# Kernel optimization log

Measured on AMD Instinct MI355X. Metric: run time of the kernel, lower is better.

Reference implementation:

```python
import jax, jax.numpy as jnp
import numpy as np

N = 50000      # nodes
E = 800000     # edges (avg degree 16)
D = 64         # num_node_features
H = 64         # hidden_channels
G = 512        # graphs in batch
OUT = 32       # final linear output
NEG_SLOPE = 0.2


def setup_inputs() -> dict:
    key = jax.random.key(0)
    ks = jax.random.split(key, 20)
    s = 0.1  # param init scale
    inp = {
        "x": jax.random.normal(ks[0], (N, D), jnp.float32),
        "edge_index": jax.random.randint(ks[1], (2, E), 0, N, dtype=jnp.int64),
        "batch": jnp.sort(jax.random.randint(ks[2], (N,), 0, G, dtype=jnp.int64)),
        # GATv2 layer 1 (D -> H)
        "Wl1": jax.random.normal(ks[3], (D, H), jnp.float32) * s,
        "bl1": jnp.zeros((H,), jnp.float32),
        "Wr1": jax.random.normal(ks[4], (D, H), jnp.float32) * s,
        "br1": jnp.zeros((H,), jnp.float32),
        "att1": jax.random.normal(ks[5], (H,), jnp.float32) * s,
        "bias1": jnp.zeros((H,), jnp.float32),
        # GATv2 layer 2 (H -> H)
        "Wl2": jax.random.normal(ks[6], (H, H), jnp.float32) * s,
        "bl2": jnp.zeros((H,), jnp.float32),
        "Wr2": jax.random.normal(ks[7], (H, H), jnp.float32) * s,
        "br2": jnp.zeros((H,), jnp.float32),
        "att2": jax.random.normal(ks[8], (H,), jnp.float32) * s,
        "bias2": jnp.zeros((H,), jnp.float32),
        # final classifier
        "lin_w": jax.random.normal(ks[9], (H, OUT), jnp.float32) * s,
        "lin_b": jnp.zeros((OUT,), jnp.float32),
    }
    return inp


def _gatv2(x, src, dst, Wl, bl, Wr, br, att, bias):
    # GATv2Conv, heads=1, PyG semantics: messages flow src -> dst
    xl = x @ Wl + bl                       # [N, H] source transform (also the message)
    xr = x @ Wr + br                       # [N, H] destination transform
    z = xl[src] + xr[dst]                  # [E, H] gather
    e = jax.nn.leaky_relu(z, NEG_SLOPE) @ att  # [E] edge scores
    # segment softmax over edges grouped by destination node
    m = jax.ops.segment_max(e, dst, num_segments=N)   # [N]
    ex = jnp.exp(e - m[dst])                          # [E]
    denom = jax.ops.segment_sum(ex, dst, num_segments=N)  # [N]
    alpha = ex / denom[dst]                            # [E]
    out = jax.ops.segment_sum(alpha[:, None] * xl[src], dst, num_segments=N)  # [N, H]
    return out + bias


def reference(x, edge_index, batch,
              Wl1, bl1, Wr1, br1, att1, bias1,
              Wl2, bl2, Wr2, br2, att2, bias2,
              lin_w, lin_b):
    src, dst = edge_index[0], edge_index[1]
    h = jax.nn.relu(_gatv2(x, src, dst, Wl1, bl1, Wr1, br1, att1, bias1))
    h = jax.nn.relu(_gatv2(h, src, dst, Wl2, bl2, Wr2, br2, att2, bias2))
    # global mean pool over graphs
    sums = jax.ops.segment_sum(h, batch, num_segments=G)          # [G, H]
    cnts = jax.ops.segment_sum(jnp.ones((h.shape[0],), h.dtype), batch, num_segments=G)
    pooled = sums / jnp.maximum(cnts, 1.0)[:, None]
    # dropout(p=0.5) is identity at inference
    return pooled @ lin_w + lin_b                                  # [G, 32]
```

## Files before the change

### kernel.cpp

```cpp
#include <hip/hip_runtime.h>
#include <hip/hip_fp16.h>
#include <math.h>


#define ELLC    48
#define OVF_CAP 65536
#define ECHUNK  2048

typedef int      vint4 __attribute__((ext_vector_type(4)));
typedef _Float16 half4 __attribute__((ext_vector_type(4)));

#define GROWS 32
__device__ __forceinline__ void dual_gemm_slim(
    int bid, int t,
    const float* __restrict__ X,
    const float* __restrict__ Wl, const float* __restrict__ bl,
    const float* __restrict__ Wr, const float* __restrict__ br,
    _Float16* __restrict__ xl, float* __restrict__ xr, int n,
    float* xS) {
    int row0 = bid * GROWS;
    for (int i = t; i < GROWS * 16; i += 256) {
        int r = row0 + (i >> 4);
        float4 v = make_float4(0.f, 0.f, 0.f, 0.f);
        if (r < n) v = ((const float4*)(X + (size_t)r * 64))[i & 15];
        ((float4*)xS)[i] = v;
    }
    __syncthreads();
    int h  = t & 63;
    int rb = t >> 6;
    float accl[8], accr[8];
#pragma unroll
    for (int i = 0; i < 8; ++i) { accl[i] = 0.f; accr[i] = 0.f; }
#pragma unroll 4
    for (int d = 0; d < 64; ++d) {
        float wl = Wl[d * 64 + h];
        float wr = Wr[d * 64 + h];
#pragma unroll
        for (int i = 0; i < 8; ++i) {
            float xv = xS[(rb + 4 * i) * 64 + d];
            accl[i] += xv * wl;
            accr[i] += xv * wr;
        }
    }
    float blv = bl[h], brv = br[h];
#pragma unroll
    for (int i = 0; i < 8; ++i) {
        int r = row0 + rb + 4 * i;
        if (r < n) {
            xl[(size_t)r * 64 + h] = (_Float16)(accl[i] + blv);
            xr[(size_t)r * 64 + h] = accr[i] + brv;
        }
    }
}

__global__ __launch_bounds__(256) void dual_gemm64_kernel(
    const float* __restrict__ X,
    const float* __restrict__ Wl, const float* __restrict__ bl,
    const float* __restrict__ Wr, const float* __restrict__ br,
    _Float16* __restrict__ xl, float* __restrict__ xr, int n) {
    __shared__ float xS[GROWS * 64];
    dual_gemm_slim(blockIdx.x, threadIdx.x, X, Wl, bl, Wr, br, xl, xr, n, xS);
}

__global__ __launch_bounds__(256) void fill_gemm_kernel(
    const int* __restrict__ src, const int* __restrict__ dst,
    int* __restrict__ cnt, unsigned short* __restrict__ ell,
    int* __restrict__ novf, int* __restrict__ ovf_dst, int* __restrict__ ovf_src,
    int E, int N, int psize, int fb,
    const float* __restrict__ X,
    const float* __restrict__ Wl, const float* __restrict__ bl,
    const float* __restrict__ Wr, const float* __restrict__ br,
    _Float16* __restrict__ xl, float* __restrict__ xr) {
    __shared__ float xS[GROWS * 64];
    int b = blockIdx.x;
    if (b >= fb) {
        dual_gemm_slim(b - fb, threadIdx.x, X, Wl, bl, Wr, br, xl, xr, N, xS);
        return;
    }
    int t     = threadIdx.x;
    int chunk = b >> 3;
    int p     = b & 7;
    int d0    = p * psize;
    int d1    = min(N, d0 + psize);
    int e0    = chunk * ECHUNK;
    int e1    = min(E, e0 + ECHUNK);
    int nq    = (e1 - e0) >> 2;
    const vint4* dst4 = (const vint4*)(dst + e0);
    const vint4* src4 = (const vint4*)(src + e0);

    auto scatter4 = [&](vint4 dv, vint4 sv) {
#pragma unroll
        for (int k = 0; k < 4; ++k) {
            int d = dv[k];
            int s = sv[k];
            if (d >= d0 && d < d1) {
                int pos = atomicAdd(&cnt[d], 1);
                if (pos < ELLC) {
                    ell[d * ELLC + pos] = (unsigned short)s;
                } else {
                    int j = atomicAdd(novf, 1);
                    if (j < OVF_CAP) { ovf_dst[j] = d; ovf_src[j] = s; }
                }
            }
        }
    };

    if (nq == (ECHUNK >> 2)) {
        vint4 dvA = __builtin_nontemporal_load(&dst4[t]);
        vint4 svA = __builtin_nontemporal_load(&src4[t]);
        vint4 dvB = __builtin_nontemporal_load(&dst4[t + 256]);
        vint4 svB = __builtin_nontemporal_load(&src4[t + 256]);
        scatter4(dvA, svA);
        scatter4(dvB, svB);
    } else {
        for (int q = t; q < nq; q += 256) {
            vint4 dv = __builtin_nontemporal_load(&dst4[q]);
            vint4 sv = __builtin_nontemporal_load(&src4[q]);
            scatter4(dv, sv);
        }
        for (int e = e0 + (nq << 2) + t; e < e1; e += 256) {
            int d = dst[e];
            if (d >= d0 && d < d1) {
                int pos = atomicAdd(&cnt[d], 1);
                int s   = src[e];
                if (pos < ELLC) {
                    ell[d * ELLC + pos] = (unsigned short)s;
                } else {
                    int j = atomicAdd(novf, 1);
                    if (j < OVF_CAP) { ovf_dst[j] = d; ovf_src[j] = s; }
                }
            }
        }
    }
}

__global__ __launch_bounds__(256) void gat_aggregate_kernel(
    const _Float16* __restrict__ xl, const float* __restrict__ xr,
    const int* __restrict__ cnt, const unsigned short* __restrict__ ell,
    const int* __restrict__ novf, const int* __restrict__ ovf_dst,
    const int* __restrict__ ovf_src,
    const float* __restrict__ att, const float* __restrict__ bias,
    float* __restrict__ out, int n) {
    int wid  = (blockIdx.x * blockDim.x + threadIdx.x) >> 6;
    int lane = threadIdx.x & 63;
    if (wid >= n) return;
    int g = lane >> 4;
    int l = lane & 15;
    int d = wid;

    float4 att4 = ((const float4*)att)[l];
    float4 b4   = ((const float4*)bias)[l];
    int deg_d = cnt[d];
    int nd  = min(deg_d, ELLC);
    int beg = d * ELLC;

    if (deg_d == 0) {
        if (g == 0) {
            float4 v;
            v.x = fmaxf(b4.x, 0.f); v.y = fmaxf(b4.y, 0.f);
            v.z = fmaxf(b4.z, 0.f); v.w = fmaxf(b4.w, 0.f);
            ((float4*)(out + (size_t)d * 64))[l] = v;
        }
        return;
    }

    int myidx = 0;
    if (lane < ELLC) myidx = (int)ell[beg + lane];
    int i_first = __shfl(myidx, 0);

    float4 xr4 = ((const float4*)(xr + (size_t)d * 64))[l];
    float  s   = 0.f;
    float4 acc = make_float4(0.f, 0.f, 0.f, 0.f);

#pragma unroll 6
    for (int k = 0; k * 8 < nd; ++k) {
        int  sa = k * 8 + g, sb = sa + 4;
        bool aa = sa < nd,   ab = sb < nd;
        int  i0 = __shfl(myidx, sa); if (!aa) i0 = i_first;
        int  i1 = __shfl(myidx, sb); if (!ab) i1 = i_first;
        half4 h0 = ((const half4*)(xl + (size_t)i0 * 64))[l];
        half4 h1 = ((const half4*)(xl + (size_t)i1 * 64))[l];
        float4 x0 = make_float4((float)h0[0], (float)h0[1], (float)h0[2], (float)h0[3]);
        float4 x1 = make_float4((float)h1[0], (float)h1[1], (float)h1[2], (float)h1[3]);
        float z, c0 = 0.f, c1 = 0.f;
        z = x0.x + xr4.x; c0 += ((z > 0.f) ? z : 0.2f * z) * att4.x;
        z = x0.y + xr4.y; c0 += ((z > 0.f) ? z : 0.2f * z) * att4.y;
        z = x0.z + xr4.z; c0 += ((z > 0.f) ? z : 0.2f * z) * att4.z;
        z = x0.w + xr4.w; c0 += ((z > 0.f) ? z : 0.2f * z) * att4.w;
        z = x1.x + xr4.x; c1 += ((z > 0.f) ? z : 0.2f * z) * att4.x;
        z = x1.y + xr4.y; c1 += ((z > 0.f) ? z : 0.2f * z) * att4.y;
        z = x1.z + xr4.z; c1 += ((z > 0.f) ? z : 0.2f * z) * att4.z;
        z = x1.w + xr4.w; c1 += ((z > 0.f) ? z : 0.2f * z) * att4.w;
#pragma unroll
        for (int sh = 8; sh >= 1; sh >>= 1) {
            c0 += __shfl_xor(c0, sh);
            c1 += __shfl_xor(c1, sh);
        }
        float w0 = aa ? __expf(fminf(c0, 30.f)) : 0.f;
        float w1 = ab ? __expf(fminf(c1, 30.f)) : 0.f;
        s += w0 + w1;
        acc.x += w0 * x0.x + w1 * x1.x;
        acc.y += w0 * x0.y + w1 * x1.y;
        acc.z += w0 * x0.z + w1 * x1.z;
        acc.w += w0 * x0.w + w1 * x1.w;
    }
    if (deg_d > ELLC) {
        int no = min(*novf, OVF_CAP);
        for (int j = g; j < no; j += 4) {
            bool active = (ovf_dst[j] == d);
            int  i0     = active ? ovf_src[j] : i_first;
            half4 h0 = ((const half4*)(xl + (size_t)i0 * 64))[l];
            float4 x0 = make_float4((float)h0[0], (float)h0[1], (float)h0[2], (float)h0[3]);
            float z, c0 = 0.f;
            z = x0.x + xr4.x; c0 += ((z > 0.f) ? z : 0.2f * z) * att4.x;
            z = x0.y + xr4.y; c0 += ((z > 0.f) ? z : 0.2f * z) * att4.y;
            z = x0.z + xr4.z; c0 += ((z > 0.f) ? z : 0.2f * z) * att4.z;
            z = x0.w + xr4.w; c0 += ((z > 0.f) ? z : 0.2f * z) * att4.w;
#pragma unroll
            for (int sh = 8; sh >= 1; sh >>= 1) c0 += __shfl_xor(c0, sh);
            float w0 = active ? __expf(fminf(c0, 30.f)) : 0.f;
            s += w0;
            acc.x += w0 * x0.x;
            acc.y += w0 * x0.y;
            acc.z += w0 * x0.z;
            acc.w += w0 * x0.w;
        }
    }
#pragma unroll
    for (int mask = 16; mask <= 32; mask <<= 1) {
        s     += __shfl_xor(s, mask);
        acc.x += __shfl_xor(acc.x, mask);
        acc.y += __shfl_xor(acc.y, mask);
        acc.z += __shfl_xor(acc.z, mask);
        acc.w += __shfl_xor(acc.w, mask);
    }
    if (g == 0) {
        float inv = (s > 0.f) ? (1.f / s) : 0.f;
        float4 v;
        v.x = fmaxf(acc.x * inv + b4.x, 0.f);
        v.y = fmaxf(acc.y * inv + b4.y, 0.f);
        v.z = fmaxf(acc.z * inv + b4.z, 0.f);
        v.w = fmaxf(acc.w * inv + b4.w, 0.f);
        ((float4*)(out + (size_t)d * 64))[l] = v;
    }
}

__global__ __launch_bounds__(256) void pool_kernel(
    const float* __restrict__ h, const int* __restrict__ batch,
    float* __restrict__ sums, float* __restrict__ cnts, int n, int nwaves) {
    int wid  = (blockIdx.x * blockDim.x + threadIdx.x) >> 6;
    int lane = threadIdx.x & 63;
    int per   = (n + nwaves - 1) / nwaves;
    int start = wid * per;
    int end   = min(n, start + per);
    if (start >= end) return;
    int cur   = batch[start];
    float acc = 0.f, cnt = 0.f;
    for (int i = start; i < end; ++i) {
        int g = batch[i];
        if (g != cur) {
            atomicAdd(&sums[cur * 64 + lane], acc);
            if (lane == 0) atomicAdd(&cnts[cur], cnt);
            acc = 0.f; cnt = 0.f; cur = g;
        }
        acc += h[(size_t)i * 64 + lane];
        cnt += 1.f;
    }
    atomicAdd(&sums[cur * 64 + lane], acc);
    if (lane == 0) atomicAdd(&cnts[cur], cnt);
}

__global__ __launch_bounds__(256) void final_kernel(
    const float* __restrict__ sums, const float* __restrict__ cnts,
    const float* __restrict__ lin_w, const float* __restrict__ lin_b,
    float* __restrict__ out, int total) {
    int tid = blockIdx.x * blockDim.x + threadIdx.x;
    if (tid >= total) return;
    int g = tid >> 5, o = tid & 31;
    float inv = 1.f / fmaxf(cnts[g], 1.f);
    float a = 0.f;
    for (int h = 0; h < 64; ++h) a += sums[g * 64 + h] * lin_w[h * 32 + o];
    out[tid] = a * inv + lin_b[o];
}

extern "C" void kernel_launch(void* const* d_in, const int* in_sizes, int n_in,
                              void* d_out, int out_size, void* d_ws, size_t ws_size,
                              hipStream_t stream) {
    const float* x     = (const float*)d_in[0];
    const int*   ei    = (const int*)d_in[1];
    const int*   batch = (const int*)d_in[2];
    const float* Wl1   = (const float*)d_in[3];
    const float* bl1   = (const float*)d_in[4];
    const float* Wr1   = (const float*)d_in[5];
    const float* br1   = (const float*)d_in[6];
    const float* att1  = (const float*)d_in[7];
    const float* bias1 = (const float*)d_in[8];
    const float* Wl2   = (const float*)d_in[9];
    const float* bl2   = (const float*)d_in[10];
    const float* Wr2   = (const float*)d_in[11];
    const float* br2   = (const float*)d_in[12];
    const float* att2  = (const float*)d_in[13];
    const float* bias2 = (const float*)d_in[14];
    const float* lin_w = (const float*)d_in[15];
    const float* lin_b = (const float*)d_in[16];
    float* out = (float*)d_out;

    const int N = in_sizes[0] / 64;
    const int E = in_sizes[1] / 2;
    const int G = out_size / 32;
    const int* src = ei;
    const int* dst = ei + E;

    char*  ws  = (char*)d_ws;
    size_t off = 0;
    auto alloc = [&](size_t bytes) -> void* {
        void* p = ws + off;
        off += bytes;
        off = (off + 255) & ~(size_t)255;
        return p;
    };
    _Float16* xl   = (_Float16*)alloc((size_t)N * 64 * sizeof(_Float16));
    float* xr      = (float*)alloc((size_t)N * 64 * sizeof(float));
    float* h1      = (float*)alloc((size_t)N * 64 * sizeof(float));
    int*   cnt     = (int*)alloc((size_t)N * sizeof(int));
    int*   novf    = (int*)alloc(256);
    float* sums    = (float*)alloc((size_t)G * 64 * sizeof(float));
    float* cnts    = (float*)alloc((size_t)G * sizeof(float));
    char*  zend    = ws + off;
    unsigned short* ell = (unsigned short*)alloc((size_t)N * ELLC * sizeof(unsigned short));
    int*   ovf_dst = (int*)alloc((size_t)OVF_CAP * sizeof(int));
    int*   ovf_src = (int*)alloc((size_t)OVF_CAP * sizeof(int));

    (void)hipMemsetAsync(cnt, 0, (size_t)(zend - (char*)cnt), stream);

    int ggrid  = (N + GROWS - 1) / GROWS;
    int agrid  = (N + 3) / 4;
    int nchunk = (E + ECHUNK - 1) / ECHUNK;
    int fb     = nchunk * 8;
    int psize  = (N + 7) / 8;

    fill_gemm_kernel<<<fb + ggrid, 256, 0, stream>>>(
        src, dst, cnt, ell, novf, ovf_dst, ovf_src, E, N, psize, fb,
        x, Wl1, bl1, Wr1, br1, xl, xr);

    gat_aggregate_kernel<<<agrid, 256, 0, stream>>>(
        xl, xr, cnt, ell, novf, ovf_dst, ovf_src, att1, bias1, h1, N);

    dual_gemm64_kernel<<<ggrid, 256, 0, stream>>>(h1, Wl2, bl2, Wr2, br2, xl, xr, N);
    gat_aggregate_kernel<<<agrid, 256, 0, stream>>>(
        xl, xr, cnt, ell, novf, ovf_dst, ovf_src, att2, bias2, h1, N);

    const int NWAVES = 2048;
    pool_kernel<<<512, 256, 0, stream>>>(h1, batch, sums, cnts, N, NWAVES);
    int total = G * 32;
    final_kernel<<<(total + 255) / 256, 256, 0, stream>>>(sums, cnts, lin_w, lin_b, out, total);
}
```

Before: 251.8 us.

## Interleave fill/GEMM blocks, persistent aggregate grid, fuse pool with final linear

Block IDs of the fused fill+GEMM kernel are now interleaved, 16 scatter blocks to 8 GEMM blocks, so both kinds of work run together instead of GEMM blocks queuing at the tail. The aggregate kernel becomes a grid-stride persistent kernel with a fixed 2048 blocks. The pool and final linear kernels are merged using a last-block ticket counter (novf+1, zeroed by the existing memset), which removes one launch. The risks are less latency hiding in the aggregate kernel and a serial final step run by a single block.

```diff
diff --git a/kernel.cpp b/kernel.cpp
--- a/kernel.cpp
+++ b/kernel.cpp
@@ -66,20 +66,25 @@
     const int* __restrict__ src, const int* __restrict__ dst,
     int* __restrict__ cnt, unsigned short* __restrict__ ell,
     int* __restrict__ novf, int* __restrict__ ovf_dst, int* __restrict__ ovf_src,
-    int E, int N, int psize, int fb,
+    int E, int N, int psize, int fb, int ggrid,
     const float* __restrict__ X,
     const float* __restrict__ Wl, const float* __restrict__ bl,
     const float* __restrict__ Wr, const float* __restrict__ br,
     _Float16* __restrict__ xl, float* __restrict__ xr) {
     __shared__ float xS[GROWS * 64];
     int b = blockIdx.x;
-    if (b >= fb) {
-        dual_gemm_slim(b - fb, threadIdx.x, X, Wl, bl, Wr, br, xl, xr, N, xS);
+    int q = b / 24, r = b % 24;
+    if (r >= 16) {
+        int vg = q * 8 + (r - 16);
+        if (vg < ggrid)
+            dual_gemm_slim(vg, threadIdx.x, X, Wl, bl, Wr, br, xl, xr, N, xS);
         return;
     }
+    int vb = q * 16 + r;
+    if (vb >= fb) return;
     int t     = threadIdx.x;
-    int chunk = b >> 3;
-    int p     = b & 7;
+    int chunk = vb >> 3;
+    int p     = vb & 7;
     int d0    = p * psize;
     int d1    = min(N, d0 + psize);
     int e0    = chunk * ECHUNK;
@@ -113,9 +118,9 @@
         scatter4(dvA, svA);
         scatter4(dvB, svB);
     } else {
-        for (int q = t; q < nq; q += 256) {
-            vint4 dv = __builtin_nontemporal_load(&dst4[q]);
-            vint4 sv = __builtin_nontemporal_load(&src4[q]);
+        for (int qq = t; qq < nq; qq += 256) {
+            vint4 dv = __builtin_nontemporal_load(&dst4[qq]);
+            vint4 sv = __builtin_nontemporal_load(&src4[qq]);
             scatter4(dv, sv);
         }
         for (int e = e0 + (nq << 2) + t; e < e1; e += 256) {
@@ -141,146 +146,155 @@
     const int* __restrict__ ovf_src,
     const float* __restrict__ att, const float* __restrict__ bias,
     float* __restrict__ out, int n) {
-    int wid  = (blockIdx.x * blockDim.x + threadIdx.x) >> 6;
+    int wid0 = (blockIdx.x * blockDim.x + threadIdx.x) >> 6;
+    int nw   = (gridDim.x * blockDim.x) >> 6;
     int lane = threadIdx.x & 63;
-    if (wid >= n) return;
     int g = lane >> 4;
     int l = lane & 15;
-    int d = wid;
-
     float4 att4 = ((const float4*)att)[l];
     float4 b4   = ((const float4*)bias)[l];
-    int deg_d = cnt[d];
-    int nd  = min(deg_d, ELLC);
-    int beg = d * ELLC;
-
-    if (deg_d == 0) {
-        if (g == 0) {
-            float4 v;
-            v.x = fmaxf(b4.x, 0.f); v.y = fmaxf(b4.y, 0.f);
-            v.z = fmaxf(b4.z, 0.f); v.w = fmaxf(b4.w, 0.f);
-            ((float4*)(out + (size_t)d * 64))[l] = v;
-        }
-        return;
-    }
-
-    int myidx = 0;
-    if (lane < ELLC) myidx = (int)ell[beg + lane];
-    int i_first = __shfl(myidx, 0);
-
-    float4 xr4 = ((const float4*)(xr + (size_t)d * 64))[l];
-    float  s   = 0.f;
-    float4 acc = make_float4(0.f, 0.f, 0.f, 0.f);
+
+    for (int d = wid0; d < n; d += nw) {
+        int deg_d = cnt[d];
+        int nd  = min(deg_d, ELLC);
+        int beg = d * ELLC;
+
+        if (deg_d == 0) {
+            if (g == 0) {
+                float4 v;
+                v.x = fmaxf(b4.x, 0.f); v.y = fmaxf(b4.y, 0.f);
+                v.z = fmaxf(b4.z, 0.f); v.w = fmaxf(b4.w, 0.f);
+                ((float4*)(out + (size_t)d * 64))[l] = v;
+            }
+            continue;
+        }
+
+        int myidx = 0;
+        if (lane < ELLC) myidx = (int)ell[beg + lane];
+        int i_first = __shfl(myidx, 0);
+
+        float4 xr4 = ((const float4*)(xr + (size_t)d * 64))[l];
+        float  s   = 0.f;
+        float4 acc = make_float4(0.f, 0.f, 0.f, 0.f);
 
 #pragma unroll 6
-    for (int k = 0; k * 8 < nd; ++k) {
-        int  sa = k * 8 + g, sb = sa + 4;
-        bool aa = sa < nd,   ab = sb < nd;
-        int  i0 = __shfl(myidx, sa); if (!aa) i0 = i_first;
-        int  i1 = __shfl(myidx, sb); if (!ab) i1 = i_first;
-        half4 h0 = ((const half4*)(xl + (size_t)i0 * 64))[l];
-        half4 h1 = ((const half4*)(xl + (size_t)i1 * 64))[l];
-        float4 x0 = make_float4((float)h0[0], (float)h0[1], (float)h0[2], (float)h0[3]);
-        float4 x1 = make_float4((float)h1[0], (float)h1[1], (float)h1[2], (float)h1[3]);
-        float z, c0 = 0.f, c1 = 0.f;
-        z = x0.x + xr4.x; c0 += ((z > 0.f) ? z : 0.2f * z) * att4.x;
-        z = x0.y + xr4.y; c0 += ((z > 0.f) ? z : 0.2f * z) * att4.y;
-        z = x0.z + xr4.z; c0 += ((z > 0.f) ? z : 0.2f * z) * att4.z;
-        z = x0.w + xr4.w; c0 += ((z > 0.f) ? z : 0.2f * z) * att4.w;
-        z = x1.x + xr4.x; c1 += ((z > 0.f) ? z : 0.2f * z) * att4.x;
-        z = x1.y + xr4.y; c1 += ((z > 0.f) ? z : 0.2f * z) * att4.y;
-        z = x1.z + xr4.z; c1 += ((z > 0.f) ? z : 0.2f * z) * att4.z;
-        z = x1.w + xr4.w; c1 += ((z > 0.f) ? z : 0.2f * z) * att4.w;
-#pragma unroll
-        for (int sh = 8; sh >= 1; sh >>= 1) {
-            c0 += __shfl_xor(c0, sh);
-            c1 += __shfl_xor(c1, sh);
-        }
-        float w0 = aa ? __expf(fminf(c0, 30.f)) : 0.f;
-        float w1 = ab ? __expf(fminf(c1, 30.f)) : 0.f;
-        s += w0 + w1;
-        acc.x += w0 * x0.x + w1 * x1.x;
-        acc.y += w0 * x0.y + w1 * x1.y;
-        acc.z += w0 * x0.z + w1 * x1.z;
-        acc.w += w0 * x0.w + w1 * x1.w;
-    }
-    if (deg_d > ELLC) {
-        int no = min(*novf, OVF_CAP);
-        for (int j = g; j < no; j += 4) {
-            bool active = (ovf_dst[j] == d);
-            int  i0     = active ? ovf_src[j] : i_first;
+        for (int k = 0; k * 8 < nd; ++k) {
+            int  sa = k * 8 + g, sb = sa + 4;
+            bool aa = sa < nd,   ab = sb < nd;
+            int  i0 = __shfl(myidx, sa); if (!aa) i0 = i_first;
+            int  i1 = __shfl(myidx, sb); if (!ab) i1 = i_first;
             half4 h0 = ((const half4*)(xl + (size_t)i0 * 64))[l];
+            half4 h1 = ((const half4*)(xl + (size_t)i1 * 64))[l];
             float4 x0 = make_float4((float)h0[0], (float)h0[1], (float)h0[2], (float)h0[3]);
-            float z, c0 = 0.f;
+            float4 x1 = make_float4((float)h1[0], (float)h1[1], (float)h1[2], (float)h1[3]);
+            float z, c0 = 0.f, c1 = 0.f;
             z = x0.x + xr4.x; c0 += ((z > 0.f) ? z : 0.2f * z) * att4.x;
             z = x0.y + xr4.y; c0 += ((z > 0.f) ? z : 0.2f * z) * att4.y;
             z = x0.z + xr4.z; c0 += ((z > 0.f) ? z : 0.2f * z) * att4.z;
             z = x0.w + xr4.w; c0 += ((z > 0.f) ? z : 0.2f * z) * att4.w;
-#pragma unroll
-            for (int sh = 8; sh >= 1; sh >>= 1) c0 += __shfl_xor(c0, sh);
-            float w0 = active ? __expf(fminf(c0, 30.f)) : 0.f;
-            s += w0;
-            acc.x += w0 * x0.x;
-            acc.y += w0 * x0.y;
-            acc.z += w0 * x0.z;
-            acc.w += w0 * x0.w;
-        }
-    }
-#pragma unroll
-    for (int mask = 16; mask <= 32; mask <<= 1) {
-        s     += __shfl_xor(s, mask);
-        acc.x += __shfl_xor(acc.x, mask);
-        acc.y += __shfl_xor(acc.y, mask);
-        acc.z += __shfl_xor(acc.z, mask);
-        acc.w += __shfl_xor(acc.w, mask);
-    }
-    if (g == 0) {
-        float inv = (s > 0.f) ? (1.f / s) : 0.f;
-        float4 v;
-        v.x = fmaxf(acc.x * inv + b4.x, 0.f);
-        v.y = fmaxf(acc.y * inv + b4.y, 0.f);
-        v.z = fmaxf(acc.z * inv + b4.z, 0.f);
-        v.w = fmaxf(acc.w * inv + b4.w, 0.f);
-        ((float4*)(out + (size_t)d * 64))[l] = v;
-    }
-}
-
-__global__ __launch_bounds__(256) void pool_kernel(
+            z = x1.x + xr4.x; c1 += ((z > 0.f) ? z : 0.2f * z) * att4.x;
+            z = x1.y + xr4.y; c1 += ((z > 0.f) ? z : 0.2f * z) * att4.y;
+            z = x1.z + xr4.z; c1 += ((z > 0.f) ? z : 0.2f * z) * att4.z;
+            z = x1.w + xr4.w; c1 += ((z > 0.f) ? z : 0.2f * z) * att4.w;
+#pragma unroll
+            for (int sh = 8; sh >= 1; sh >>= 1) {
+                c0 += __shfl_xor(c0, sh);
+                c1 += __shfl_xor(c1, sh);
+            }
+            float w0 = aa ? __expf(fminf(c0, 30.f)) : 0.f;
+            float w1 = ab ? __expf(fminf(c1, 30.f)) : 0.f;
+            s += w0 + w1;
+            acc.x += w0 * x0.x + w1 * x1.x;
+            acc.y += w0 * x0.y + w1 * x1.y;
+            acc.z += w0 * x0.z + w1 * x1.z;
+            acc.w += w0 * x0.w + w1 * x1.w;
+        }
+        if (deg_d > ELLC) {
+            int no = min(*novf, OVF_CAP);
+            for (int j = g; j < no; j += 4) {
+                bool active = (ovf_dst[j] == d);
+                int  i0     = active ? ovf_src[j] : i_first;
+                half4 h0 = ((const half4*)(xl + (size_t)i0 * 64))[l];
+                float4 x0 = make_float4((float)h0[0], (float)h0[1], (float)h0[2], (float)h0[3]);
+                float z, c0 = 0.f;
+                z = x0.x + xr4.x; c0 += ((z > 0.f) ? z : 0.2f * z) * att4.x;
+                z = x0.y + xr4.y; c0 += ((z > 0.f) ? z : 0.2f * z) * att4.y;
+                z = x0.z + xr4.z; c0 += ((z > 0.f) ? z : 0.2f * z) * att4.z;
+                z = x0.w + xr4.w; c0 += ((z > 0.f) ? z : 0.2f * z) * att4.w;
+#pragma unroll
+                for (int sh = 8; sh >= 1; sh >>= 1) c0 += __shfl_xor(c0, sh);
+                float w0 = active ? __expf(fminf(c0, 30.f)) : 0.f;
+                s += w0;
+                acc.x += w0 * x0.x;
+                acc.y += w0 * x0.y;
+                acc.z += w0 * x0.z;
+                acc.w += w0 * x0.w;
+            }
+        }
+#pragma unroll
+        for (int mask = 16; mask <= 32; mask <<= 1) {
+            s     += __shfl_xor(s, mask);
+            acc.x += __shfl_xor(acc.x, mask);
+            acc.y += __shfl_xor(acc.y, mask);
+            acc.z += __shfl_xor(acc.z, mask);
+            acc.w += __shfl_xor(acc.w, mask);
+        }
+        if (g == 0) {
+            float inv = (s > 0.f) ? (1.f / s) : 0.f;
+            float4 v;
+            v.x = fmaxf(acc.x * inv + b4.x, 0.f);
+            v.y = fmaxf(acc.y * inv + b4.y, 0.f);
+            v.z = fmaxf(acc.z * inv + b4.z, 0.f);
+            v.w = fmaxf(acc.w * inv + b4.w, 0.f);
+            ((float4*)(out + (size_t)d * 64))[l] = v;
+        }
+    }
+}
+
+__global__ __launch_bounds__(256) void pool_final_kernel(
     const float* __restrict__ h, const int* __restrict__ batch,
-    float* __restrict__ sums, float* __restrict__ cnts, int n, int nwaves) {
-    int wid  = (blockIdx.x * blockDim.x + threadIdx.x) >> 6;
-    int lane = threadIdx.x & 63;
-    int per   = (n + nwaves - 1) / nwaves;
-    int start = wid * per;
-    int end   = min(n, start + per);
-    if (start >= end) return;
-    int cur   = batch[start];
-    float acc = 0.f, cnt = 0.f;
-    for (int i = start; i < end; ++i) {
-        int g = batch[i];
-        if (g != cur) {
+    float* __restrict__ sums, float* __restrict__ cnts, int n, int nwaves,
+    int* __restrict__ done,
+    const float* __restrict__ lin_w, const float* __restrict__ lin_b,
+    float* __restrict__ out, int G) {
+    __shared__ int ticketS;
+    {
+        int wid  = (blockIdx.x * blockDim.x + threadIdx.x) >> 6;
+        int lane = threadIdx.x & 63;
+        int per   = (n + nwaves - 1) / nwaves;
+        int start = wid * per;
+        int end   = min(n, start + per);
+        if (start < end) {
+            int cur   = batch[start];
+            float acc = 0.f, cnt = 0.f;
+            for (int i = start; i < end; ++i) {
+                int g = batch[i];
+                if (g != cur) {
+                    atomicAdd(&sums[cur * 64 + lane], acc);
+                    if (lane == 0) atomicAdd(&cnts[cur], cnt);
+                    acc = 0.f; cnt = 0.f; cur = g;
+                }
+                acc += h[(size_t)i * 64 + lane];
+                cnt += 1.f;
+            }
             atomicAdd(&sums[cur * 64 + lane], acc);
             if (lane == 0) atomicAdd(&cnts[cur], cnt);
-            acc = 0.f; cnt = 0.f; cur = g;
-        }
-        acc += h[(size_t)i * 64 + lane];
-        cnt += 1.f;
-    }
-    atomicAdd(&sums[cur * 64 + lane], acc);
-    if (lane == 0) atomicAdd(&cnts[cur], cnt);
-}
-
-__global__ __launch_bounds__(256) void final_kernel(
-    const float* __restrict__ sums, const float* __restrict__ cnts,
-    const float* __restrict__ lin_w, const float* __restrict__ lin_b,
-    float* __restrict__ out, int total) {
-    int tid = blockIdx.x * blockDim.x + threadIdx.x;
-    if (tid >= total) return;
-    int g = tid >> 5, o = tid & 31;
-    float inv = 1.f / fmaxf(cnts[g], 1.f);
-    float a = 0.f;
-    for (int h = 0; h < 64; ++h) a += sums[g * 64 + h] * lin_w[h * 32 + o];
-    out[tid] = a * inv + lin_b[o];
+        }
+    }
+    __threadfence();
+    __syncthreads();
+    if (threadIdx.x == 0) ticketS = atomicAdd(done, 1);
+    __syncthreads();
+    if (ticketS != (int)gridDim.x - 1) return;
+    __threadfence();
+    for (int i = threadIdx.x; i < G * 32; i += 256) {
+        int g = i >> 5, o = i & 31;
+        float inv = 1.f / fmaxf(cnts[g], 1.f);
+        float a = 0.f;
+#pragma unroll 8
+        for (int hh = 0; hh < 64; ++hh) a += sums[g * 64 + hh] * lin_w[hh * 32 + o];
+        out[i] = a * inv + lin_b[o];
+    }
 }
 
 extern "C" void kernel_launch(void* const* d_in, const int* in_sizes, int n_in,
@@ -334,13 +348,15 @@
     (void)hipMemsetAsync(cnt, 0, (size_t)(zend - (char*)cnt), stream);
 
     int ggrid  = (N + GROWS - 1) / GROWS;
-    int agrid  = (N + 3) / 4;
     int nchunk = (E + ECHUNK - 1) / ECHUNK;
     int fb     = nchunk * 8;
     int psize  = (N + 7) / 8;
-
-    fill_gemm_kernel<<<fb + ggrid, 256, 0, stream>>>(
-        src, dst, cnt, ell, novf, ovf_dst, ovf_src, E, N, psize, fb,
+    int ngroups = max((fb + 15) / 16, (ggrid + 7) / 8);
+    int igrid   = ngroups * 24;
+    int agrid   = 2048;
+
+    fill_gemm_kernel<<<igrid, 256, 0, stream>>>(
+        src, dst, cnt, ell, novf, ovf_dst, ovf_src, E, N, psize, fb, ggrid,
         x, Wl1, bl1, Wr1, br1, xl, xr);
 
     gat_aggregate_kernel<<<agrid, 256, 0, stream>>>(
@@ -351,7 +367,6 @@
         xl, xr, cnt, ell, novf, ovf_dst, ovf_src, att2, bias2, h1, N);
 
     const int NWAVES = 2048;
-    pool_kernel<<<512, 256, 0, stream>>>(h1, batch, sums, cnts, N, NWAVES);
-    int total = G * 32;
-    final_kernel<<<(total + 255) / 256, 256, 0, stream>>>(sums, cnts, lin_w, lin_b, out, total);
-}
+    pool_final_kernel<<<512, 256, 0, stream>>>(h1, batch, sums, cnts, N, NWAVES,
+                                               novf + 1, lin_w, lin_b, out, G);
+}
```

After: 380.9 us. 1.51x slower.
